# Performance work log

Measured on AMD Instinct MI355X. Metric: run time of the kernel, lower is better.

Reference implementation:

```python
import jax, jax.numpy as jnp
import numpy as np

B, S, H = 32, 512, 768
NH, HD = 8, 96
NC = 3
SEP = 102
NEG = -1e9


def telu(x):
    return x * jnp.tanh(jnp.exp(x))


def setup_inputs() -> dict:
    rng = np.random.default_rng(0)
    key = jax.random.key(0)
    ks = jax.random.split(key, 16)
    # ragged premise/hypothesis spans: [CLS] premise [SEP] hypothesis [SEP] pad
    s1 = rng.integers(64, 256, size=B)
    s2 = rng.integers(s1 + 32, 500)
    ids = rng.integers(1000, 30000, size=(B, S))  # avoid accidental SEP ids
    for i in range(B):
        ids[i, 0] = 101
        ids[i, s1[i]] = SEP
        ids[i, s2[i]] = SEP
        ids[i, s2[i] + 1:] = 0
    pos = np.arange(S)[None, :]
    am = (pos <= s2[:, None]).astype(np.int32)

    def lin(k, i, o):
        return jax.random.normal(k, (i, o), jnp.float32) * 0.02

    return dict(
        hidden_states=jax.random.normal(ks[0], (B, S, H), jnp.float32),
        input_ids=jnp.asarray(ids, jnp.int32),
        attention_mask=jnp.asarray(am, jnp.int32),
        fe_w1=lin(ks[1], H, 512), fe_b1=jnp.zeros(512), fe_g=jnp.ones(512), fe_be=jnp.zeros(512),
        fe_w2=lin(ks[2], 512, 128), fe_b2=jnp.zeros(128),
        al_w1=lin(ks[3], 2 * H, 768), al_b1=jnp.zeros(768),
        al_w2=lin(ks[4], 768, 128), al_b2=jnp.zeros(128),
        mha_wq=lin(ks[5], H, H), mha_bq=jnp.zeros(H),
        mha_wk=lin(ks[6], H, H), mha_bk=jnp.zeros(H),
        mha_wv=lin(ks[7], H, H), mha_bv=jnp.zeros(H),
        mha_wo=lin(ks[8], H, H), mha_bo=jnp.zeros(H),
        dp_w=lin(ks[9], H, 128), dp_b=jnp.zeros(128),
        ap_w=lin(ks[10], H, 128), ap_b=jnp.zeros(128),
        cl_w1=lin(ks[11], 512, 64), cl_b1=jnp.zeros(64),
        cl_w2=lin(ks[12], 64, NC), cl_b2=jnp.zeros(NC),
    )


def reference(hidden_states, input_ids, attention_mask,
              fe_w1, fe_b1, fe_g, fe_be, fe_w2, fe_b2,
              al_w1, al_b1, al_w2, al_b2,
              mha_wq, mha_bq, mha_wk, mha_bk, mha_wv, mha_bv, mha_wo, mha_bo,
              dp_w, dp_b, ap_w, ap_b, cl_w1, cl_b1, cl_w2, cl_b2):
    hs = hidden_states
    am = attention_mask.astype(hs.dtype)
    sep = (input_ids == SEP)
    pos = jnp.arange(S)[None, :]
    s1 = jnp.argmax(sep, axis=1)            # first SEP
    s2 = (S - 1) - jnp.argmax(sep[:, ::-1], axis=1)  # second SEP
    prem = ((pos >= 1) & (pos < s1[:, None])).astype(hs.dtype)   # premise span [1, s1)
    hyp = ((pos > s1[:, None]) & (pos < s2[:, None])).astype(hs.dtype)  # hypothesis (s1, s2)

    def mmean(x, m):  # masked mean over seq: x [B,S,H], m [B,S]
        return jnp.einsum('bsh,bs->bh', x, m) / jnp.clip(m.sum(1, keepdims=True), 1e-9, None)

    # pooled + mean + max representations -> feature_extractor
    pooled = hs[:, 0]
    mean_rep = mmean(hs, am)
    max_rep = jnp.max(jnp.where(am[..., None] > 0, hs, NEG), axis=1)
    h = (pooled + mean_rep + max_rep) @ fe_w1 + fe_b1
    h = (h - h.mean(-1, keepdims=True)) / jnp.sqrt(h.var(-1, keepdims=True) + 1e-5) * fe_g + fe_be
    feat = telu(h @ fe_w2 + fe_b2)

    # sentence diff head
    sent_diff = jnp.abs(mmean(hs, prem) - mmean(hs, hyp))
    diff_rep = telu(sent_diff @ dp_w + dp_b)

    # cross attention: hypothesis queries attend to premise keys/values
    q = (hs @ mha_wq + mha_bq).reshape(B, S, NH, HD)
    k = (hs @ mha_wk + mha_bk).reshape(B, S, NH, HD)
    v = (hs @ mha_wv + mha_bv).reshape(B, S, NH, HD)
    scores = jnp.einsum('bqhd,bkhd->bhqk', q, k) / np.sqrt(HD).astype(np.float32)
    scores = jnp.where(prem[:, None, None, :] > 0, scores, NEG)
    attn = jax.nn.softmax(scores, axis=-1)
    ctx = jnp.einsum('bhqk,bkhd->bqhd', attn, v).reshape(B, S, H) @ mha_wo + mha_bo
    attn_rep = telu(mmean(ctx, hyp) @ ap_w + ap_b)

    # word alignment (both directions share one similarity matrix)
    sim = jnp.einsum('bsd,btd->bst', hs, hs)
    w_p2h = jax.nn.softmax(jnp.where(hyp[:, None, :] > 0, sim, NEG), axis=-1)
    al1 = mmean(jnp.einsum('bst,btd->bsd', w_p2h, hs), prem)
    w_h2p = jax.nn.softmax(jnp.where(prem[:, None, :] > 0, sim, NEG), axis=-1)
    al2 = mmean(jnp.einsum('bst,btd->bsd', w_h2p, hs), hyp)
    align_rep = telu((jnp.concatenate([al1, al2], -1) @ al_w1 + al_b1) @ al_w2 + al_b2)

    combined = jnp.concatenate([feat, diff_rep, attn_rep, align_rep], -1)  # [B, 512]
    logits = telu(combined @ cl_w1 + cl_b1) @ cl_w2 + cl_b2
    return logits
```

## Files before the change

### kernel.cpp

```cpp
#include <hip/hip_runtime.h>
#include <hip/hip_bf16.h>
#include <math.h>

#define SS 512
#define HH 768
#define NEGV -1e9f
#define APAD 100

typedef float f32x4 __attribute__((ext_vector_type(4)));
typedef __bf16 bf16x8 __attribute__((ext_vector_type(8)));

__device__ __forceinline__ float telu_f(float x){ return x * tanhf(expf(x)); }

__device__ __forceinline__ short f2bf(float x){
  __hip_bfloat16 h = __float2bfloat16(x);
  return __builtin_bit_cast(short, h);
}
__device__ __forceinline__ float b2f(short s){
  __hip_bfloat16 h = __builtin_bit_cast(__hip_bfloat16, s);
  return __bfloat162float(h);
}

__device__ __forceinline__ void gl_lds16(const void* g, void* l){
  __builtin_amdgcn_global_load_lds((const __attribute__((address_space(1))) void*)g,
                                   (__attribute__((address_space(3))) void*)l, 16, 0, 0);
}

__device__ __forceinline__ float wred_max(float v){
  #pragma unroll
  for (int o=32;o>0;o>>=1) v = fmaxf(v, __shfl_xor(v, o));
  return v;
}
__device__ __forceinline__ float wred_sum(float v){
  #pragma unroll
  for (int o=32;o>0;o>>=1) v += __shfl_xor(v, o);
  return v;
}

__global__ __launch_bounds__(512) void k_scan(const int* __restrict__ ids, const int* __restrict__ am,
                       int* s1a, int* s2a, float* invnam, float* invnp, float* invnh,
                       float* __restrict__ uacc, float* __restrict__ v1g, float* __restrict__ v2g){
  int b = blockIdx.x, tid = threadIdx.x;
  __shared__ int mn, mx, cnt;
  if (tid==0){ mn = 1<<30; mx = -1; cnt = 0; }
  __syncthreads();
  int id = ids[b*SS+tid];
  if (id==102){ atomicMin(&mn, tid); atomicMax(&mx, tid); }
  atomicAdd(&cnt, am[b*SS+tid]);
  #pragma unroll
  for (int i=0;i<4;i++) uacc[(size_t)b*2048 + tid + i*512] = 0.f;
  v1g[b*SS+tid] = 0.f;
  v2g[b*SS+tid] = 0.f;
  __syncthreads();
  if (tid==0){
    int s1 = mn; if (s1 > 255) s1 = 255; if (s1 < 1) s1 = 1;
    int s2 = mx; if (s2 < s1+1) s2 = s1+1; if (s2 > 511) s2 = 511;
    s1a[b]=s1; s2a[b]=s2;
    invnam[b] = 1.f/fmaxf((float)cnt, 1e-9f);
    invnp[b]  = 1.f/fmaxf((float)(s1-1), 1e-9f);
    invnh[b]  = 1.f/fmaxf((float)(s2-s1-1), 1e-9f);
  }
}

__global__ __launch_bounds__(256) void k_g2(const float* __restrict__ hs, const int* __restrict__ amask,
    const int* __restrict__ s1a, const int* __restrict__ s2a,
    short* __restrict__ hsb, short* __restrict__ hsl, float4* __restrict__ repp,
    const float* __restrict__ wq, const float* __restrict__ wk, const float* __restrict__ wv,
    short* __restrict__ Wt){
  __shared__ __align__(16) char smem[16896];
  int id = blockIdx.x, tid = threadIdx.x;
  if (id < 768){
    int b = id&31, hc = (id>>5)%6, sc = id/192;
    int* ams = (int*)smem;
    float4* rb4 = (float4*)(smem + 512);
    int sbase = sc*128;
    if (tid < 128) ams[tid] = amask[b*SS + sbase + tid];
    __syncthreads();
    int s1 = s1a[b], s2 = s2a[b];
    int hlane = tid & 31, srow = tid >> 5;
    int h0 = hc*128 + hlane*4;
    float sm[4]={0,0,0,0}, sp[4]={0,0,0,0}, sh[4]={0,0,0,0};
    float mxv[4]={NEGV,NEGV,NEGV,NEGV};
    for (int si = srow; si < 128; si += 8){
      int s = sbase + si;
      float4 x = *(const float4*)(hs + ((size_t)(b*SS+s))*HH + h0);
      float xv[4] = {x.x,x.y,x.z,x.w};
      bool am = ams[si] > 0;
      bool ip = (s>=1 && s<s1), ih = (s>s1 && s<s2);
      short hi4[4], lo4[4];
      #pragma unroll
      for (int c=0;c<4;c++){
        if (am){ sm[c]+=xv[c]; mxv[c]=fmaxf(mxv[c],xv[c]); }
        if (ip) sp[c]+=xv[c];
        if (ih) sh[c]+=xv[c];
        hi4[c] = f2bf(xv[c]);
        lo4[c] = f2bf(xv[c] - b2f(hi4[c]));
      }
      *(short4*)(hsb + ((size_t)(b*SS+s))*HH + h0) = *(short4*)hi4;
      *(short4*)(hsl + ((size_t)(b*SS+s))*HH + h0) = *(short4*)lo4;
    }
    #pragma unroll
    for (int c=0;c<4;c++) rb4[srow*128 + hlane*4+c] = make_float4(sm[c], mxv[c], sp[c], sh[c]);
    __syncthreads();
    if (tid < 128){
      float4 a = rb4[tid];
      #pragma unroll
      for (int r=1;r<8;r++){
        float4 v = rb4[r*128 + tid];
        a.x += v.x; a.y = fmaxf(a.y, v.y); a.z += v.z; a.w += v.w;
      }
      repp[(((size_t)(b*6+hc))*4 + sc)*128 + tid] = a;
    }
  } else {
    int w = id - 768;
    int k0 = (w%24)*32, n0 = ((w/24)%24)*32, which = w/576;
    const float* W = which==0? wq : (which==1? wk : wv);
    float (*tl)[33] = (float(*)[33])smem;
    int r = tid>>3, c4 = (tid&7)*4;
    float4 v = *(const float4*)(W + (size_t)(k0+r)*HH + n0 + c4);
    tl[r][c4+0]=v.x; tl[r][c4+1]=v.y; tl[r][c4+2]=v.z; tl[r][c4+3]=v.w;
    __syncthreads();
    short4 o;
    o.x = f2bf(tl[c4+0][r]); o.y = f2bf(tl[c4+1][r]);
    o.z = f2bf(tl[c4+2][r]); o.w = f2bf(tl[c4+3][r]);
    *(short4*)(Wt + (size_t)which*HH*HH + (size_t)(n0+r)*HH + k0 + c4) = o;
  }
}

__device__ __forceinline__ void build_vec(const float4* __restrict__ repp, const float* __restrict__ hs,
    const float* __restrict__ invnam, const float* __restrict__ invnp, const float* __restrict__ invnh,
    int b, int tid, bool want_sdiff, float* xs){
  for (int h = tid; h < HH; h += 256){
    int hc = h>>7, hr = h&127;
    float S=0.f, M=NEGV, P=0.f, Hh=0.f;
    #pragma unroll
    for (int sc=0; sc<4; sc++){
      float4 v = repp[(((size_t)(b*6+hc))*4 + sc)*128 + hr];
      S += v.x; M = fmaxf(M, v.y); P += v.z; Hh += v.w;
    }
    if (want_sdiff) xs[h] = fabsf(P*invnp[b] - Hh*invnh[b]);
    else            xs[h] = hs[((size_t)(b*SS))*HH + h] + S*invnam[b] + M;
  }
}

__global__ __launch_bounds__(256) void k_mm(const short* __restrict__ hsb, const short* __restrict__ hsl,
    const short* __restrict__ Wt,
    const float* __restrict__ bq, const float* __restrict__ bk, const float* __restrict__ bv,
    short* __restrict__ qbh, short* __restrict__ kbh, float* __restrict__ vb,
    const int* __restrict__ s1a, const int* __restrict__ s2a, float* __restrict__ sim,
    const float4* __restrict__ repp, const float* __restrict__ hs,
    const float* __restrict__ invnam, const float* __restrict__ invnp, const float* __restrict__ invnh,
    const float* __restrict__ fe_w1, const float* __restrict__ fe_b1, float* __restrict__ featd,
    const float* __restrict__ dpw, const float* __restrict__ dpb, float* __restrict__ comb){
  __shared__ __align__(16) short smem_s[32768];
  int id = blockIdx.x;
  int tid = threadIdx.x, lane = tid&63, wave = tid>>6;
  int wm = wave>>1, wn = wave&1;
  int lm = lane&15, lq = lane>>4;
  if (id < 512){
    int local = id;
    int b = (local&7) + 8*(local>>7);
    int t = (local>>3)&15;
    int s0 = (t>>2)*128, t0 = (t&3)*128;
    int s2 = s2a[b];
    if (s0 >= s2 || t0 >= s2) return;
    const size_t base = (size_t)b*SS*HH;
    auto stage = [&](int k0, int bufi){
      short* Ah = smem_s + bufi*16384;
      short* Al = Ah + 4096;
      short* Bh = Ah + 8192;
      short* Bl = Ah + 12288;
      #pragma unroll
      for (int t2=0;t2<2;t2++){
        int c = tid + t2*256;
        int ib = c>>6, l = c&63;
        int row = ib*16 + (l&15);
        int kk  = k0 + (l>>4)*8;
        gl_lds16(hsb + base + (size_t)(s0+row)*HH + kk, Ah + c*8);
        gl_lds16(hsl + base + (size_t)(s0+row)*HH + kk, Al + c*8);
        gl_lds16(hsb + base + (size_t)(t0+row)*HH + kk, Bh + c*8);
        gl_lds16(hsl + base + (size_t)(t0+row)*HH + kk, Bl + c*8);
      }
    };
    f32x4 acc[4][4];
    #pragma unroll
    for (int i=0;i<4;i++)
      #pragma unroll
      for (int j=0;j<4;j++) acc[i][j] = (f32x4){0.f,0.f,0.f,0.f};
    stage(0, 0);
    __syncthreads();
    int bufi = 0;
    for (int k0=0;k0<HH;k0+=32){
      if (k0+32 < HH) stage(k0+32, bufi^1);
      short* Ah = smem_s + bufi*16384;
      short* Al = Ah + 4096;
      short* Bh = Ah + 8192;
      short* Bl = Ah + 12288;
      bf16x8 ah[4], al[4], bh[4], bl[4];
      #pragma unroll
      for (int i=0;i<4;i++){
        ah[i] = *(const bf16x8*)&Ah[((wm*4+i)*64 + lane)*8];
        al[i] = *(const bf16x8*)&Al[((wm*4+i)*64 + lane)*8];
      }
      #pragma unroll
      for (int j=0;j<4;j++){
        bh[j] = *(const bf16x8*)&Bh[((wn*4+j)*64 + lane)*8];
        bl[j] = *(const bf16x8*)&Bl[((wn*4+j)*64 + lane)*8];
      }
      #pragma unroll
      for (int i=0;i<4;i++)
        #pragma unroll
        for (int j=0;j<4;j++){
          acc[i][j] = __builtin_amdgcn_mfma_f32_16x16x32_bf16(ah[i], bh[j], acc[i][j], 0, 0, 0);
          acc[i][j] = __builtin_amdgcn_mfma_f32_16x16x32_bf16(ah[i], bl[j], acc[i][j], 0, 0, 0);
          acc[i][j] = __builtin_amdgcn_mfma_f32_16x16x32_bf16(al[i], bh[j], acc[i][j], 0, 0, 0);
        }
      __syncthreads();
      bufi ^= 1;
    }
    #pragma unroll
    for (int i=0;i<4;i++){
      #pragma unroll
      for (int j=0;j<4;j++){
        int col = t0 + wn*64 + j*16 + lm;
        #pragma unroll
        for (int r4=0;r4<4;r4++){
          int row = s0 + wm*64 + i*16 + lq*4 + r4;
          sim[((size_t)(b*SS+row))*SS + col] = acc[i][j][r4];
        }
      }
    }
  } else if (id < 2048){
    int which, local;
    int qid = id - 512;
    if (qid < 768){ which=0; local=qid; }
    else if (qid < 1152){ which=1; local=qid-768; }
    else { which=2; local=qid-1152; }
    int r8 = local & 7, n = (local>>3)%6, gq = local/48;
    int rt = gq*8 + r8;
    int n0 = n*128;
    int r0, b;
    if (which==0){ r0 = rt*128; b = r0>>9; }
    else { b = rt>>1; r0 = b*512 + (rt&1)*128; }
    int s1 = s1a[b], s2 = s2a[b];
    int s0 = r0 & (SS-1);
    if (which==0){ if (s0 >= s2 || s0 + 127 <= s1) return; }
    else { if (s0 >= s1) return; }
    const float* bias = which==0? bq : (which==1? bk : bv);
    const short* Wb = Wt + (size_t)which*HH*HH;
    auto stageq = [&](int k0, int bufi){
      short* As = smem_s + bufi*8192;
      short* Bs = As + 4096;
      #pragma unroll
      for (int t2=0;t2<2;t2++){
        int c = tid + t2*256;
        int ib = c>>6, l = c&63;
        int row = ib*16 + (l&15);
        int kk  = k0 + (l>>4)*8;
        gl_lds16(hsb + (size_t)(r0+row)*HH + kk, As + c*8);
        gl_lds16(Wb  + (size_t)(n0+row)*HH + kk, Bs + c*8);
      }
    };
    f32x4 acc[4][4];
    #pragma unroll
    for (int i=0;i<4;i++)
      #pragma unroll
      for (int j=0;j<4;j++) acc[i][j] = (f32x4){0.f,0.f,0.f,0.f};
    stageq(0, 0);
    __syncthreads();
    int bufi = 0;
    for (int k0=0;k0<HH;k0+=32){
      if (k0+32 < HH) stageq(k0+32, bufi^1);
      short* As = smem_s + bufi*8192;
      short* Bs = As + 4096;
      bf16x8 af[4], bfv[4];
      #pragma unroll
      for (int i=0;i<4;i++) af[i]  = *(const bf16x8*)&As[((wm*4+i)*64 + lane)*8];
      #pragma unroll
      for (int j=0;j<4;j++) bfv[j] = *(const bf16x8*)&Bs[((wn*4+j)*64 + lane)*8];
      #pragma unroll
      for (int i=0;i<4;i++)
        #pragma unroll
        for (int j=0;j<4;j++)
          acc[i][j] = __builtin_amdgcn_mfma_f32_16x16x32_bf16(af[i], bfv[j], acc[i][j], 0, 0, 0);
      __syncthreads();
      bufi ^= 1;
    }
    #pragma unroll
    for (int i=0;i<4;i++){
      #pragma unroll
      for (int j=0;j<4;j++){
        int col = n0 + wn*64 + j*16 + lm;
        float bcol = bias[col];
        #pragma unroll
        for (int r4=0;r4<4;r4++){
          int row = r0 + wm*64 + i*16 + lq*4 + r4;
          int s = row & (SS-1);
          float val = acc[i][j][r4] + bcol;
          if (which==0){
            if (s > s1 && s < s2) qbh[(size_t)row*HH + col] = f2bf(val);
          } else if (s >= 1 && s < s1){
            size_t o = ((size_t)(b*256+s))*HH + col;
            if (which==1) kbh[o] = f2bf(val); else vb[o] = val;
          }
        }
      }
    }
  } else {
    int sid = id - 2048;
    float* xs = (float*)smem_s;
    float* psum = xs + HH;
    int jj = tid & 127, half = tid >> 7;
    if (sid < 128){
      int b = sid&31, j0 = (sid>>5)*128;
      build_vec(repp, hs, invnam, invnp, invnh, b, tid, false, xs);
      __syncthreads();
      float a = 0.f;
      #pragma unroll 8
      for (int i = half*384; i < half*384+384; i++)
        a += xs[i]*fe_w1[(size_t)i*512 + j0 + jj];
      psum[half*128 + jj] = a;
      __syncthreads();
      if (tid < 128)
        featd[(size_t)b*512 + j0 + tid] = fe_b1[j0+tid] + psum[tid] + psum[128+tid];
    } else {
      int b = sid - 128;
      build_vec(repp, hs, invnam, invnp, invnh, b, tid, true, xs);
      __syncthreads();
      float a = 0.f;
      #pragma unroll 8
      for (int i = half*384; i < half*384+384; i++)
        a += xs[i]*dpw[(size_t)i*128 + jj];
      psum[half*128 + jj] = a;
      __syncthreads();
      if (tid < 128)
        comb[b*512 + 128 + tid] = telu_f(dpb[tid] + psum[tid] + psum[128+tid]);
    }
  }
}

__global__ __launch_bounds__(256) void k_attn_simsm(const short* __restrict__ qbh, const short* __restrict__ kbh,
    const int* __restrict__ s1a, const int* __restrict__ s2a, float* __restrict__ uacc,
    const float* __restrict__ sim, float* __restrict__ v1g, float* __restrict__ v2g){
  __shared__ __align__(16) char smem[64000];
  int id = blockIdx.x, tid = threadIdx.x;
  int wave = tid>>6, lane = tid&63;
  if (id < 2048){
    int b = id&31, h = (id>>5)&7, zc = id>>8;
    int s1 = s1a[b], s2 = s2a[b];
    int qs = s1 + 1 + zc*64;
    if (qs >= s2) return;
    short* Ks = (short*)smem;
    short* Qs = Ks + 256*APAD;
    int lm = lane&15, lq = lane>>4;
    int jmax = (s1+15)>>4;
    int krows = jmax<<4;
    for (int i = tid; i < krows*12; i += 256){
      int r = i/12, c = i - r*12;
      *(int4*)&Ks[r*APAD + c*8] = *(const int4*)(kbh + ((size_t)(b*256+r))*HH + h*96 + c*8);
    }
    for (int i = tid; i < 64*12; i += 256){
      int r = i/12, c = i - r*12;
      int q = qs + r;
      int4 v = {0,0,0,0};
      if (q < SS) v = *(const int4*)(qbh + ((size_t)(b*SS+q))*HH + h*96 + c*8);
      *(int4*)&Qs[r*APAD + c*8] = v;
    }
    __syncthreads();
    f32x4 acc[16];
    #pragma unroll
    for (int j=0;j<16;j++) acc[j] = (f32x4){0.f,0.f,0.f,0.f};
    #pragma unroll
    for (int ks=0; ks<3; ks++){
      bf16x8 a = *(const bf16x8*)&Qs[(wave*16+lm)*APAD + ks*32 + lq*8];
      #pragma unroll
      for (int j=0;j<16;j++){
        if (j < jmax){
          bf16x8 bfr = *(const bf16x8*)&Ks[(j*16+lm)*APAD + ks*32 + lq*8];
          acc[j] = __builtin_amdgcn_mfma_f32_16x16x32_bf16(a, bfr, acc[j], 0, 0, 0);
        }
      }
    }
    const float scale = 0.1020620726f;
    float uj[16];
    #pragma unroll
    for (int j=0;j<16;j++) uj[j]=0.f;
    int qrow_base = qs + wave*16 + lq*4;
    #pragma unroll
    for (int r=0;r<4;r++){
      float m = -1e30f;
      float sc[16];
      #pragma unroll
      for (int j=0;j<16;j++){
        int c = j*16 + lm;
        float s = (c>=1 && c<s1) ? acc[j][r]*scale : -1e30f;
        sc[j] = s; m = fmaxf(m, s);
      }
      #pragma unroll
      for (int o=1;o<16;o<<=1) m = fmaxf(m, __shfl_xor(m, o));
      float ssum = 0.f;
      #pragma unroll
      for (int j=0;j<16;j++){ float p = expf(sc[j]-m); sc[j]=p; ssum += p; }
      #pragma unroll
      for (int o=1;o<16;o<<=1) ssum += __shfl_xor(ssum, o);
      bool rvalid = (qrow_base + r) < s2;
      float inv = rvalid ? 1.f/ssum : 0.f;
      #pragma unroll
      for (int j=0;j<16;j++) uj[j] += sc[j]*inv;
    }
    #pragma unroll
    for (int j=0;j<16;j++){
      if (j < jmax){
        float v = uj[j];
        v += __shfl_xor(v, 16);
        v += __shfl_xor(v, 32);
        if (lq==0 && v != 0.f)
          atomicAdd(&uacc[((size_t)(b*8+h))*256 + j*16 + lm], v);
      }
    }
  } else {
    int l = id - 2048;
    int b = l&31, cy = l>>5;
    int s1 = s1a[b], s2 = s2a[b];
    int r0 = cy*64;
    float* av = (float*)smem;
    for (int i=tid;i<2*4*SS;i+=256) av[i]=0.f;
    __syncthreads();
    for (int r = r0 + wave; r < r0+64; r += 4){
      int t0,t1,which;
      if (r>=1 && r<s1){ t0=s1+1; t1=s2; which=0; }
      else if (r>s1 && r<s2){ t0=1; t1=s1; which=1; }
      else continue;
      const float* row = sim + ((size_t)(b*SS+r))*SS;
      float vals[7]; float mx=-1e30f;
      #pragma unroll
      for (int j=0;j<7;j++){
        int t = t0 + lane + 64*j;
        vals[j] = (t<t1) ? row[t] : -1e30f;
        mx = fmaxf(mx, vals[j]);
      }
      mx = wred_max(mx);
      float ssum=0.f;
      #pragma unroll
      for (int j=0;j<7;j++){
        int t = t0+lane+64*j;
        vals[j] = (t<t1)? expf(vals[j]-mx) : 0.f;
        ssum += vals[j];
      }
      ssum = wred_sum(ssum);
      float inv = 1.f/ssum;
      #pragma unroll
      for (int j=0;j<7;j++){
        int t = t0+lane+64*j;
        if (t<t1) av[(which*4 + wave)*SS + t] += vals[j]*inv;
      }
    }
    __syncthreads();
    for (int t=tid;t<SS;t+=256){
      float a0 = av[0*SS+t]+av[1*SS+t]+av[2*SS+t]+av[3*SS+t];
      float a1 = av[4*SS+t]+av[5*SS+t]+av[6*SS+t]+av[7*SS+t];
      if (a0 != 0.f) atomicAdd(&v1g[b*SS+t], a0);
      if (a1 != 0.f) atomicAdd(&v2g[b*SS+t], a1);
    }
  }
}

__global__ __launch_bounds__(256) void k_ctx_alvec(const float* __restrict__ uacc, const float* __restrict__ vb,
    const int* __restrict__ s1a, const float* __restrict__ invnh, float* __restrict__ cmg,
    const float* __restrict__ hs, const float* __restrict__ v1g, const float* __restrict__ v2g,
    const float* __restrict__ invnp, float* __restrict__ catg){
  __shared__ __align__(16) char smem[9216];
  int id = blockIdx.x, tid = threadIdx.x;
  if (id < 192){
    int b = id&31, i0 = (id>>5)*128;
    int s1 = s1a[b]; int nk = s1-1;
    float inh = invnh[b];
    float* us = (float*)smem;
    float* ps = us + 2048;
    for (int idx=tid; idx<2048; idx+=256) us[idx] = uacc[(size_t)b*2048 + idx];
    __syncthreads();
    int ii = tid & 127, half = tid >> 7;
    int i = i0 + ii;
    int h = i/96;
    float a = 0.f;
    int lo = 1 + half*128;
    int hi = nk < (lo+127) ? nk : (lo+127);
    for (int sl=lo; sl<=hi; sl++)
      a += us[h*256+sl]*vb[((size_t)(b*256+sl))*HH + i];
    ps[half*128 + ii] = a;
    __syncthreads();
    if (tid < 128)
      cmg[(size_t)b*HH + i0 + tid] = (ps[tid] + ps[128+tid])*inh;
  } else {
    int l = id - 192;
    int b = l&31, d0 = (l>>5)*64;
    float* sv1 = (float*)smem;
    float* sv2 = sv1 + 512;
    float* p1  = sv2 + 512;
    float* p2  = p1 + 256;
    for (int t=tid;t<SS;t+=256){ sv1[t]=v1g[b*SS+t]; sv2[t]=v2g[b*SS+t]; }
    __syncthreads();
    int d = d0 + (tid&63), ch = tid>>6;
    float a1=0.f, a2=0.f;
    for (int t=ch*128; t<ch*128+128; t++){
      float x = hs[((size_t)(b*SS+t))*HH + d];
      a1 += sv1[t]*x; a2 += sv2[t]*x;
    }
    p1[ch*64 + (tid&63)]=a1; p2[ch*64 + (tid&63)]=a2;
    __syncthreads();
    if (tid < 64){
      float s1_ = p1[tid]+p1[64+tid]+p1[128+tid]+p1[192+tid];
      float s2_ = p2[tid]+p2[64+tid]+p2[128+tid]+p2[192+tid];
      catg[(size_t)b*1536 + d0 + tid]       = s1_*invnp[b];
      catg[(size_t)b*1536 + 768 + d0 + tid] = s2_*invnh[b];
    }
  }
}

template<int K>
__device__ __forceinline__ void gemv_ct(const float* __restrict__ x, const float* __restrict__ W,
    const float* __restrict__ bias, float* __restrict__ y, int b, int j0, int tid,
    float* xs, float* psum){
  for (int i=tid;i<K;i+=256) xs[i] = x[(size_t)b*K + i];
  __syncthreads();
  int jj = tid & 127, half = tid >> 7;
  int j = j0 + jj;
  float a = 0.f;
  #pragma unroll 8
  for (int i = half*(K/2); i < (half+1)*(K/2); i++)
    a += xs[i]*W[(size_t)i*HH + j];
  psum[half*128 + jj] = a;
  __syncthreads();
  if (tid < 128)
    y[(size_t)b*HH + j0 + tid] = bias[j0+tid] + psum[tid] + psum[128+tid];
}

__global__ __launch_bounds__(256) void k_gemvB(const float* __restrict__ cmg, const float* __restrict__ wo,
    const float* __restrict__ bo, float* __restrict__ accg,
    const float* __restrict__ catg, const float* __restrict__ al_w1, const float* __restrict__ al_b1,
    float* __restrict__ tmpg){
  __shared__ float xs[1536];
  __shared__ float psum[256];
  int id = blockIdx.x, tid = threadIdx.x;
  if (id < 192){
    gemv_ct<768>(cmg, wo, bo, accg, id&31, (id>>5)*128, tid, xs, psum);
  } else {
    int l = id-192;
    gemv_ct<1536>(catg, al_w1, al_b1, tmpg, l&31, (l>>5)*128, tid, xs, psum);
  }
}

__global__ __launch_bounds__(256) void k_tailsC(const float* __restrict__ accg, const float* __restrict__ apw,
    const float* __restrict__ apb, const float* __restrict__ tmpg, const float* __restrict__ al_w2,
    const float* __restrict__ al_b2, float* __restrict__ comb,
    const float* __restrict__ featd, const float* __restrict__ g, const float* __restrict__ be,
    const float* __restrict__ w2, const float* __restrict__ b2){
  __shared__ __align__(16) float smem[1664];
  int id = blockIdx.x, tid = threadIdx.x;
  if (id < 64){
    float* xs = smem;
    float* psum = smem + HH;
    const float *x, *W, *bias; int b, off;
    if (id < 32){ b = id; x=accg; W=apw; bias=apb; off=256; }
    else { b = id-32; x=tmpg; W=al_w2; bias=al_b2; off=384; }
    for (int i=tid;i<HH;i+=256) xs[i] = x[(size_t)b*HH + i];
    __syncthreads();
    int jj = tid & 127, half = tid >> 7;
    float a = 0.f;
    #pragma unroll 8
    for (int i = half*384; i < half*384+384; i++)
      a += xs[i]*W[(size_t)i*128 + jj];
    psum[half*128 + jj] = a;
    __syncthreads();
    if (tid < 128)
      comb[b*512 + off + tid] = telu_f(bias[tid] + psum[tid] + psum[128+tid]);
  } else {
    int b = id - 64;
    float* hv  = smem;
    float* hn  = hv + 512;
    float* red = hn + 512;
    float* ps  = red + 256;
    hv[tid] = featd[(size_t)b*512 + tid];
    hv[tid+256] = featd[(size_t)b*512 + tid + 256];
    __syncthreads();
    red[tid] = hv[tid] + hv[tid+256];
    __syncthreads();
    for (int st=128; st>0; st>>=1){ if (tid<st) red[tid]+=red[tid+st]; __syncthreads(); }
    float mean = red[0]*(1.f/512.f);
    __syncthreads();
    float d0 = hv[tid]-mean, d1 = hv[tid+256]-mean;
    red[tid] = d0*d0 + d1*d1;
    __syncthreads();
    for (int st=128; st>0; st>>=1){ if (tid<st) red[tid]+=red[tid+st]; __syncthreads(); }
    float inv = 1.f/sqrtf(red[0]*(1.f/512.f) + 1e-5f);
    __syncthreads();
    hn[tid]     = d0*inv*g[tid]     + be[tid];
    hn[tid+256] = d1*inv*g[tid+256] + be[tid+256];
    __syncthreads();
    int jj = tid & 127, half = tid >> 7;
    float a = 0.f;
    #pragma unroll 8
    for (int k = half*256; k < half*256+256; k++)
      a += hn[k]*w2[k*128 + jj];
    ps[half*128 + jj] = a;
    __syncthreads();
    if (tid < 128)
      comb[b*512 + tid] = telu_f(b2[tid] + ps[tid] + ps[128+tid]);
  }
}

__global__ __launch_bounds__(64) void k_cls(const float* __restrict__ comb,
    const float* __restrict__ w1, const float* __restrict__ b1,
    const float* __restrict__ w2, const float* __restrict__ b2, float* __restrict__ out){
  int b=blockIdx.x, tid=threadIdx.x;
  __shared__ float cb[512];
  __shared__ float t1[64];
  for (int i=tid;i<512;i+=64) cb[i]=comb[b*512+i];
  __syncthreads();
  float a = b1[tid];
  for (int k=0;k<512;k++) a += cb[k]*w1[(size_t)k*64+tid];
  t1[tid]=telu_f(a);
  __syncthreads();
  if (tid<3){
    float o = b2[tid];
    for (int k=0;k<64;k++) o += t1[k]*w2[k*3+tid];
    out[b*3+tid]=o;
  }
}

extern "C" void kernel_launch(void* const* d_in, const int* in_sizes, int n_in,
                              void* d_out, int out_size, void* d_ws, size_t ws_size,
                              hipStream_t stream){
  const float* hs   = (const float*)d_in[0];
  const int*   ids  = (const int*)d_in[1];
  const int*   amask= (const int*)d_in[2];
  const float* fe_w1= (const float*)d_in[3];
  const float* fe_b1= (const float*)d_in[4];
  const float* fe_g = (const float*)d_in[5];
  const float* fe_be= (const float*)d_in[6];
  const float* fe_w2= (const float*)d_in[7];
  const float* fe_b2= (const float*)d_in[8];
  const float* al_w1= (const float*)d_in[9];
  const float* al_b1= (const float*)d_in[10];
  const float* al_w2= (const float*)d_in[11];
  const float* al_b2= (const float*)d_in[12];
  const float* wq   = (const float*)d_in[13];
  const float* bq   = (const float*)d_in[14];
  const float* wk   = (const float*)d_in[15];
  const float* bk   = (const float*)d_in[16];
  const float* wv   = (const float*)d_in[17];
  const float* bv   = (const float*)d_in[18];
  const float* wo   = (const float*)d_in[19];
  const float* bo   = (const float*)d_in[20];
  const float* dpw  = (const float*)d_in[21];
  const float* dpb  = (const float*)d_in[22];
  const float* apw  = (const float*)d_in[23];
  const float* apb  = (const float*)d_in[24];
  const float* clw1 = (const float*)d_in[25];
  const float* clb1 = (const float*)d_in[26];
  const float* clw2 = (const float*)d_in[27];
  const float* clb2 = (const float*)d_in[28];
  float* out = (float*)d_out;

  char* base = (char*)d_ws;
  size_t off = 0;
  auto alloc = [&](size_t bytes)->char*{ char* p = base + off; off += (bytes + 255) & ~(size_t)255; return p; };
  short* hsb  = (short*)alloc((size_t)32*SS*HH*2);
  short* hsl  = (short*)alloc((size_t)32*SS*HH*2);
  short* Wt   = (short*)alloc((size_t)3*HH*HH*2);
  short* qbh  = (short*)alloc((size_t)32*SS*HH*2);
  short* kbh  = (short*)alloc((size_t)32*256*HH*2);
  float* vb   = (float*)alloc((size_t)32*256*HH*4);
  float* simb = (float*)alloc((size_t)32*SS*SS*4);
  float* uacc = (float*)alloc((size_t)32*8*256*4);
  float* v1g  = (float*)alloc((size_t)32*SS*4);
  float* v2g  = (float*)alloc((size_t)32*SS*4);
  int*   s1a  = (int*)alloc(32*4);
  int*   s2a  = (int*)alloc(32*4);
  float* invnam=(float*)alloc(32*4);
  float* invnp =(float*)alloc(32*4);
  float* invnh =(float*)alloc(32*4);
  float* comb = (float*)alloc((size_t)32*512*4);
  float4* repp= (float4*)alloc((size_t)32*6*4*128*16);
  float* featd= (float*)alloc((size_t)32*512*4);
  float* catg = (float*)alloc((size_t)32*1536*4);
  float* tmpg = (float*)alloc((size_t)32*HH*4);
  float* cmg  = (float*)alloc((size_t)32*HH*4);
  float* accg = (float*)alloc((size_t)32*HH*4);

  k_scan<<<dim3(32), dim3(512), 0, stream>>>(ids, amask, s1a, s2a, invnam, invnp, invnh, uacc, v1g, v2g);
  k_g2<<<dim3(2496), dim3(256), 0, stream>>>(hs, amask, s1a, s2a, hsb, hsl, repp, wq, wk, wv, Wt);
  k_mm<<<dim3(2208), dim3(256), 0, stream>>>(hsb, hsl, Wt, bq, bk, bv, qbh, kbh, vb, s1a, s2a, simb,
                                             repp, hs, invnam, invnp, invnh, fe_w1, fe_b1, featd, dpw, dpb, comb);
  k_attn_simsm<<<dim3(2304), dim3(256), 0, stream>>>(qbh, kbh, s1a, s2a, uacc, simb, v1g, v2g);
  k_ctx_alvec<<<dim3(576), dim3(256), 0, stream>>>(uacc, vb, s1a, invnh, cmg, hs, v1g, v2g, invnp, catg);
  k_gemvB<<<dim3(384), dim3(256), 0, stream>>>(cmg, wo, bo, accg, catg, al_w1, al_b1, tmpg);
  k_tailsC<<<dim3(96), dim3(256), 0, stream>>>(accg, apw, apb, tmpg, al_w2, al_b2, comb,
                                               featd, fe_g, fe_be, fe_w2, fe_b2);
  k_cls<<<dim3(32), dim3(64), 0, stream>>>(comb, clw1, clb1, clw2, clb2, out);
}
```

Before: 510.4 us.

## Exploit symmetry of similarity matrix and halve LDS footprint in k_mm

The hs·hsᵀ similarity GEMM now computes only the upper-triangular 128x128 tiles (10 of 16 per batch) and writes each off-diagonal tile twice, once transposed. Diagonal tiles load a single operand and reuse it for both sides. The QKV GEMM swaps its double-buffered prefetch for single-stage loads of 64-wide K chunks, which halves shared memory to 32KB and should let more blocks share a CU. The catch is that loads no longer overlap with MFMA work, and the transposed stores go to strided rows.

```diff
diff --git a/kernel.cpp b/kernel.cpp
--- a/kernel.cpp
+++ b/kernel.cpp
@@ -152,24 +152,33 @@
     const float* __restrict__ invnam, const float* __restrict__ invnp, const float* __restrict__ invnh,
     const float* __restrict__ fe_w1, const float* __restrict__ fe_b1, float* __restrict__ featd,
     const float* __restrict__ dpw, const float* __restrict__ dpb, float* __restrict__ comb){
-  __shared__ __align__(16) short smem_s[32768];
+  __shared__ __align__(16) short smem_s[16384];
   int id = blockIdx.x;
   int tid = threadIdx.x, lane = tid&63, wave = tid>>6;
   int wm = wave>>1, wn = wave&1;
   int lm = lane&15, lq = lane>>4;
-  if (id < 512){
-    int local = id;
-    int b = (local&7) + 8*(local>>7);
-    int t = (local>>3)&15;
-    int s0 = (t>>2)*128, t0 = (t&3)*128;
+  if (id < 320){
+    const int TI[10]={0,0,0,0,1,1,1,2,2,3};
+    const int TJ[10]={0,1,2,3,1,2,3,2,3,3};
+    int b8 = id & 7, q = id >> 3;
+    int t = q % 10, bhi = q / 10;
+    int b = b8 + 8*bhi;
+    int s0 = TI[t]*128, t0 = TJ[t]*128;
     int s2 = s2a[b];
-    if (s0 >= s2 || t0 >= s2) return;
+    if (t0 >= s2) return;
+    bool diag = (s0 == t0);
+    short* Ah = smem_s;
+    short* Al = Ah + 4096;
+    short* Bh = diag ? Ah : (Ah + 8192);
+    short* Bl = diag ? Al : (Ah + 12288);
     const size_t base = (size_t)b*SS*HH;
-    auto stage = [&](int k0, int bufi){
-      short* Ah = smem_s + bufi*16384;
-      short* Al = Ah + 4096;
-      short* Bh = Ah + 8192;
-      short* Bl = Ah + 12288;
+    f32x4 acc[4][4];
+    #pragma unroll
+    for (int i=0;i<4;i++)
+      #pragma unroll
+      for (int j=0;j<4;j++) acc[i][j] = (f32x4){0.f,0.f,0.f,0.f};
+    for (int k0=0;k0<HH;k0+=32){
+      __syncthreads();
       #pragma unroll
       for (int t2=0;t2<2;t2++){
         int c = tid + t2*256;
@@ -178,24 +187,12 @@
         int kk  = k0 + (l>>4)*8;
         gl_lds16(hsb + base + (size_t)(s0+row)*HH + kk, Ah + c*8);
         gl_lds16(hsl + base + (size_t)(s0+row)*HH + kk, Al + c*8);
-        gl_lds16(hsb + base + (size_t)(t0+row)*HH + kk, Bh + c*8);
-        gl_lds16(hsl + base + (size_t)(t0+row)*HH + kk, Bl + c*8);
-      }
-    };
-    f32x4 acc[4][4];
-    #pragma unroll
-    for (int i=0;i<4;i++)
-      #pragma unroll
-      for (int j=0;j<4;j++) acc[i][j] = (f32x4){0.f,0.f,0.f,0.f};
-    stage(0, 0);
-    __syncthreads();
-    int bufi = 0;
-    for (int k0=0;k0<HH;k0+=32){
-      if (k0+32 < HH) stage(k0+32, bufi^1);
-      short* Ah = smem_s + bufi*16384;
-      short* Al = Ah + 4096;
-      short* Bh = Ah + 8192;
-      short* Bl = Ah + 12288;
+        if (!diag){
+          gl_lds16(hsb + base + (size_t)(t0+row)*HH + kk, Bh + c*8);
+          gl_lds16(hsl + base + (size_t)(t0+row)*HH + kk, Bl + c*8);
+        }
+      }
+      __syncthreads();
       bf16x8 ah[4], al[4], bh[4], bl[4];
       #pragma unroll
       for (int i=0;i<4;i++){
@@ -215,8 +212,6 @@
           acc[i][j] = __builtin_amdgcn_mfma_f32_16x16x32_bf16(ah[i], bl[j], acc[i][j], 0, 0, 0);
           acc[i][j] = __builtin_amdgcn_mfma_f32_16x16x32_bf16(al[i], bh[j], acc[i][j], 0, 0, 0);
         }
-      __syncthreads();
-      bufi ^= 1;
     }
     #pragma unroll
     for (int i=0;i<4;i++){
@@ -230,9 +225,21 @@
         }
       }
     }
-  } else if (id < 2048){
+    if (!diag){
+      #pragma unroll
+      for (int i=0;i<4;i++){
+        #pragma unroll
+        for (int j=0;j<4;j++){
+          int col  = t0 + wn*64 + j*16 + lm;
+          int row0 = s0 + wm*64 + i*16 + lq*4;
+          float4 v; v.x=acc[i][j][0]; v.y=acc[i][j][1]; v.z=acc[i][j][2]; v.w=acc[i][j][3];
+          *(float4*)(sim + ((size_t)(b*SS+col))*SS + row0) = v;
+        }
+      }
+    }
+  } else if (id < 1856){
     int which, local;
-    int qid = id - 512;
+    int qid = id - 320;
     if (qid < 768){ which=0; local=qid; }
     else if (qid < 1152){ which=1; local=qid-768; }
     else { which=2; local=qid-1152; }
@@ -248,43 +255,48 @@
     else { if (s0 >= s1) return; }
     const float* bias = which==0? bq : (which==1? bk : bv);
     const short* Wb = Wt + (size_t)which*HH*HH;
-    auto stageq = [&](int k0, int bufi){
-      short* As = smem_s + bufi*8192;
-      short* Bs = As + 4096;
+    short* As0 = smem_s;
+    short* Bs0 = As0 + 4096;
+    short* As1 = As0 + 8192;
+    short* Bs1 = As0 + 12288;
+    f32x4 acc[4][4];
+    #pragma unroll
+    for (int i=0;i<4;i++)
+      #pragma unroll
+      for (int j=0;j<4;j++) acc[i][j] = (f32x4){0.f,0.f,0.f,0.f};
+    for (int k0=0;k0<HH;k0+=64){
+      __syncthreads();
       #pragma unroll
       for (int t2=0;t2<2;t2++){
         int c = tid + t2*256;
         int ib = c>>6, l = c&63;
         int row = ib*16 + (l&15);
-        int kk  = k0 + (l>>4)*8;
-        gl_lds16(hsb + (size_t)(r0+row)*HH + kk, As + c*8);
-        gl_lds16(Wb  + (size_t)(n0+row)*HH + kk, Bs + c*8);
-      }
-    };
-    f32x4 acc[4][4];
-    #pragma unroll
-    for (int i=0;i<4;i++)
-      #pragma unroll
-      for (int j=0;j<4;j++) acc[i][j] = (f32x4){0.f,0.f,0.f,0.f};
-    stageq(0, 0);
-    __syncthreads();
-    int bufi = 0;
-    for (int k0=0;k0<HH;k0+=32){
-      if (k0+32 < HH) stageq(k0+32, bufi^1);
-      short* As = smem_s + bufi*8192;
-      short* Bs = As + 4096;
+        int kk  = (l>>4)*8;
+        gl_lds16(hsb + (size_t)(r0+row)*HH + k0 + kk,      As0 + c*8);
+        gl_lds16(Wb  + (size_t)(n0+row)*HH + k0 + kk,      Bs0 + c*8);
+        gl_lds16(hsb + (size_t)(r0+row)*HH + k0 + 32 + kk, As1 + c*8);
+        gl_lds16(Wb  + (size_t)(n0+row)*HH + k0 + 32 + kk, Bs1 + c*8);
+      }
+      __syncthreads();
       bf16x8 af[4], bfv[4];
       #pragma unroll
-      for (int i=0;i<4;i++) af[i]  = *(const bf16x8*)&As[((wm*4+i)*64 + lane)*8];
-      #pragma unroll
-      for (int j=0;j<4;j++) bfv[j] = *(const bf16x8*)&Bs[((wn*4+j)*64 + lane)*8];
+      for (int i=0;i<4;i++) af[i]  = *(const bf16x8*)&As0[((wm*4+i)*64 + lane)*8];
+      #pragma unroll
+      for (int j=0;j<4;j++) bfv[j] = *(const bf16x8*)&Bs0[((wn*4+j)*64 + lane)*8];
       #pragma unroll
       for (int i=0;i<4;i++)
         #pragma unroll
         for (int j=0;j<4;j++)
           acc[i][j] = __builtin_amdgcn_mfma_f32_16x16x32_bf16(af[i], bfv[j], acc[i][j], 0, 0, 0);
-      __syncthreads();
-      bufi ^= 1;
+      #pragma unroll
+      for (int i=0;i<4;i++) af[i]  = *(const bf16x8*)&As1[((wm*4+i)*64 + lane)*8];
+      #pragma unroll
+      for (int j=0;j<4;j++) bfv[j] = *(const bf16x8*)&Bs1[((wn*4+j)*64 + lane)*8];
+      #pragma unroll
+      for (int i=0;i<4;i++)
+        #pragma unroll
+        for (int j=0;j<4;j++)
+          acc[i][j] = __builtin_amdgcn_mfma_f32_16x16x32_bf16(af[i], bfv[j], acc[i][j], 0, 0, 0);
     }
     #pragma unroll
     for (int i=0;i<4;i++){
@@ -307,7 +319,7 @@
       }
     }
   } else {
-    int sid = id - 2048;
+    int sid = id - 1856;
     float* xs = (float*)smem_s;
     float* psum = xs + HH;
     int jj = tid & 127, half = tid >> 7;
@@ -690,7 +702,7 @@
 
   k_scan<<<dim3(32), dim3(512), 0, stream>>>(ids, amask, s1a, s2a, invnam, invnp, invnh, uacc, v1g, v2g);
   k_g2<<<dim3(2496), dim3(256), 0, stream>>>(hs, amask, s1a, s2a, hsb, hsl, repp, wq, wk, wv, Wt);
-  k_mm<<<dim3(2208), dim3(256), 0, stream>>>(hsb, hsl, Wt, bq, bk, bv, qbh, kbh, vb, s1a, s2a, simb,
+  k_mm<<<dim3(2016), dim3(256), 0, stream>>>(hsb, hsl, Wt, bq, bk, bv, qbh, kbh, vb, s1a, s2a, simb,
                                              repp, hs, invnam, invnp, invnh, fe_w1, fe_b1, featd, dpw, dpb, comb);
   k_attn_simsm<<<dim3(2304), dim3(256), 0, stream>>>(qbh, kbh, s1a, s2a, uacc, simb, v1g, v2g);
   k_ctx_alvec<<<dim3(576), dim3(256), 0, stream>>>(uacc, vb, s1a, invnh, cmg, hs, v1g, v2g, invnp, catg);
```

Result: faster. 478.5 us (-6.3%).
